# Kernel optimization log

Hardware: AMD Instinct MI355X
Metric: run time of the kernel (lower is better)

Reference implementation:

```python
import jax, jax.numpy as jnp
import numpy as np

B, S, D, H, IT, V = 2, 1024, 1024, 8, 28, 50257
DH = D // H
EPS = jnp.float32(1.1920929e-07)  # torch RMSNorm default eps = finfo(float32).eps


def _rmsnorm(x, w):
    # torch nn.RMSNorm: x * rsqrt(mean(x^2) + eps) * weight
    ms = jnp.mean(jnp.square(x), axis=-1, keepdims=True)
    return x * jax.lax.rsqrt(ms + EPS) * w


def setup_inputs() -> dict:
    key = jax.random.key(0)
    ks = jax.random.split(key, 8)
    s = 0.02
    tokens = jax.random.randint(ks[0], (B, S), 0, V)
    embed = jax.random.normal(ks[1], (V, D), dtype=jnp.float32) * s
    Wk = jax.random.normal(ks[2], (D, D), dtype=jnp.float32) * s
    Wv = jax.random.normal(ks[3], (D, D), dtype=jnp.float32) * s
    Ws = jax.random.normal(ks[4], (D, D), dtype=jnp.float32) * s
    Wo = jax.random.normal(ks[5], (D, D), dtype=jnp.float32) * s  # original zero-inits; randomized for a non-trivial baseline
    step_size = jnp.linspace(0.5, 0.1, IT, dtype=jnp.float32)
    norm_w = jnp.ones((IT, D), jnp.float32)   # per-iteration RMSNorm weight
    gamma = jnp.ones((IT, D), jnp.float32)
    beta = jnp.zeros((IT, D), jnp.float32)
    out_norm_w = jnp.ones((D,), jnp.float32)
    lm_head_w = jax.random.normal(ks[6], (V, D), dtype=jnp.float32) * s
    return dict(tokens=tokens, embed=embed, Wk=Wk, Wv=Wv, Ws=Ws, Wo=Wo,
                step_size=step_size, norm_w=norm_w, gamma=gamma, beta=beta,
                out_norm_w=out_norm_w, lm_head_w=lm_head_w)


def _forward(tokens, embed, Wk, Wv, Ws, Wo, step_size, norm_w, gamma, beta, out_norm_w, lm_head_w):
    b, s = tokens.shape
    causal = jnp.tril(jnp.ones((s, s), dtype=bool))  # allow j <= i
    scale = 1.0 / np.sqrt(DH)

    def compute_force(h):
        k = (h @ Wk.T).reshape(b, s, H, DH)
        v = (h @ Wv.T).reshape(b, s, H, DH)
        energy = jnp.einsum('bihd,bjhd->bhij', k, k) * scale
        logits = jnp.where(causal, -energy, -jnp.inf)  # softmax(-energy) with causal masking
        w = jax.nn.softmax(logits, axis=-1)
        pairwise = jnp.einsum('bhij,bjhd->bihd', w, v).reshape(b, s, D)
        return (pairwise + h @ Ws.T) @ Wo.T

    def step(x, p):
        st, nw, g, bb = p
        h = _rmsnorm(x, nw) * g + bb
        return x + compute_force(h) * st, None

    x0 = embed[tokens].astype(jnp.float32)
    x, _ = jax.lax.scan(jax.checkpoint(step), x0, (step_size, norm_w, gamma, beta))
    x = _rmsnorm(x, out_norm_w)
    return x @ lm_head_w.T  # [B, S, V] logits


def reference(tokens, embed, Wk, Wv, Ws, Wo, step_size, norm_w, gamma, beta, out_norm_w, lm_head_w):
    return _forward(tokens, embed, Wk, Wv, Ws, Wo, step_size, norm_w, gamma, beta, out_norm_w, lm_head_w)
```

## Files before the change

### kernel.cpp

```cpp
#include <hip/hip_runtime.h>
#include <cstdint>
#include <cstddef>

#define S_   1024
#define D_   1024
#define H_   8
#define DH_  128
#define IT_  28
#define V_   50257
#define B_   2
#define ROWS 2048
#define EPS_ 1.1920929e-07f

typedef unsigned short u16;
typedef __attribute__((ext_vector_type(8))) short s8v;
typedef __attribute__((ext_vector_type(4))) float f4v;

#define VMCNT0 asm volatile("s_waitcnt vmcnt(0)" ::: "memory")
#define RBAR   do { __builtin_amdgcn_s_barrier(); asm volatile("" ::: "memory"); } while (0)

static __device__ __forceinline__ void gload16(const void* g, void* l) {
  __builtin_amdgcn_global_load_lds((__attribute__((address_space(1))) void*)(g),
                                   (__attribute__((address_space(3))) void*)(l), 16, 0, 0);
}

static __device__ __forceinline__ u16 f2bf(float f) {
  union { float f; uint32_t u; } v; v.f = f;
  return (u16)((v.u + 0x7FFFu + ((v.u >> 16) & 1u)) >> 16);
}

static __device__ __forceinline__ float wave_sum(float v) {
#pragma unroll
  for (int o = 32; o > 0; o >>= 1) v += __shfl_xor(v, o, 64);
  return v;
}

__device__ __constant__ int IT_TAB[40] = {
  15,15,15,15, 14,14,14, 13,13,13, 12,12,12, 11,11,11,
  10,10, 9,9, 8,8, 7,7, 6, 5, 4, 3,
  14,10,6,2, 13,9,5,1, 12,8,4,0};
__device__ __constant__ int CH_TAB[40] = {
  0,1,2,3, 0,1,2, 0,1,2, 0,1,2, 0,1,2,
  0,1, 0,1, 0,1, 0,1, 0, 0, 0, 0,
  3,2,1,0, 3,2,1,0, 3,2,1,0};

__global__ __launch_bounds__(256) void k_embed(const int* __restrict__ tok,
                                               const float* __restrict__ emb,
                                               float* __restrict__ x) {
  const int row = blockIdx.x;
  const int t = tok[row];
  ((float4*)(x + (size_t)row * D_))[threadIdx.x] =
      ((const float4*)(emb + (size_t)t * D_))[threadIdx.x];
}

__global__ __launch_bounds__(256) void k_cvt(const float* __restrict__ w,
                                             u16* __restrict__ o, int n4) {
  const int idx = blockIdx.x * 256 + threadIdx.x;
  if (idx < n4) {
    const float4 f = ((const float4*)w)[idx];
    ushort4 u;
    u.x = f2bf(f.x); u.y = f2bf(f.y); u.z = f2bf(f.z); u.w = f2bf(f.w);
    ((ushort4*)o)[idx] = u;
  }
}

__global__ __launch_bounds__(256) void k_rmsnorm(const float* __restrict__ x,
                                                 const float* __restrict__ nw,
                                                 const float* __restrict__ g,
                                                 const float* __restrict__ bb,
                                                 u16* __restrict__ h) {
  const int row = blockIdx.x;
  const int tid = threadIdx.x;
  const float4 xv = ((const float4*)(x + (size_t)row * D_))[tid];
  float ss = xv.x*xv.x + xv.y*xv.y + xv.z*xv.z + xv.w*xv.w;
  ss = wave_sum(ss);
  __shared__ float red[4];
  const int lane = tid & 63, wid = tid >> 6;
  if (lane == 0) red[wid] = ss;
  __syncthreads();
  const float tot = red[0] + red[1] + red[2] + red[3];
  const float r = rsqrtf(tot * (1.0f / (float)D_) + EPS_);
  const float4 wv = ((const float4*)nw)[tid];
  float o[4];
  o[0] = xv.x * r * wv.x; o[1] = xv.y * r * wv.y;
  o[2] = xv.z * r * wv.z; o[3] = xv.w * r * wv.w;
  if (g) {
    const float4 gv = ((const float4*)g)[tid];
    const float4 bv = ((const float4*)bb)[tid];
    o[0] = o[0]*gv.x + bv.x; o[1] = o[1]*gv.y + bv.y;
    o[2] = o[2]*gv.z + bv.z; o[3] = o[3]*gv.w + bv.w;
  }
  ushort4 u;
  u.x = f2bf(o[0]); u.y = f2bf(o[1]); u.z = f2bf(o[2]); u.w = f2bf(o[3]);
  ((ushort4*)(h + (size_t)row * D_))[tid] = u;
}


__global__ __launch_bounds__(256) void k_gemm2(const u16* __restrict__ A, int lda,
                                               const u16* __restrict__ Bm, int ldb,
                                               float* __restrict__ C, int ldc,
                                               int K,
                                               const float* __restrict__ alphap, int aidx) {
  __shared__ u16 As0[128 * 32], As1[128 * 32];
  __shared__ u16 Bs0[64 * 32], Bs1[64 * 32];
  const int wk = (blockIdx.x & 7) * (gridDim.x >> 3) + (blockIdx.x >> 3);
  const int i0 = (wk & 15) * 128;
  const int j0 = (wk >> 4) * 64;
  const int tid = threadIdx.x;
  const int lane = tid & 63, w = tid >> 6;
  const int wr = w >> 1, wc = w & 1;
  const int l15 = lane & 15, l4 = lane >> 4;
  const int ar = tid >> 2;
  const int ak = (((tid & 3) ^ ((ar >> 1) & 3)) << 3);
  const int sw = (l15 >> 1) & 3;

  f4v acc[4][2];
#pragma unroll
  for (int m = 0; m < 4; ++m)
#pragma unroll
    for (int n = 0; n < 2; ++n) acc[m][n] = (f4v)0.0f;

  auto STAGE = [&](u16* AsB, u16* BsB, int k0) {
    gload16(A + (size_t)(i0 + ar) * lda + k0 + ak, AsB + (size_t)tid * 8);
    gload16(A + (size_t)(i0 + ar + 64) * lda + k0 + ak, AsB + ((size_t)tid + 256) * 8);
    gload16(Bm + (size_t)(j0 + ar) * ldb + k0 + ak, BsB + (size_t)tid * 8);
  };
  auto COMP = [&](const u16* AsB, const u16* BsB) {
    s8v a[4], b[2];
#pragma unroll
    for (int m = 0; m < 4; ++m)
      a[m] = *(const s8v*)&AsB[(wr * 64 + m * 16 + l15) * 32 + ((l4 ^ sw) << 3)];
#pragma unroll
    for (int n = 0; n < 2; ++n)
      b[n] = *(const s8v*)&BsB[(wc * 32 + n * 16 + l15) * 32 + ((l4 ^ sw) << 3)];
#pragma unroll
    for (int m = 0; m < 4; ++m)
#pragma unroll
      for (int n = 0; n < 2; ++n)
        acc[m][n] = __builtin_amdgcn_mfma_f32_16x16x32_bf16(a[m], b[n], acc[m][n], 0, 0, 0);
  };

  STAGE(As0, Bs0, 0);
  VMCNT0;
  RBAR;
  for (int k0 = 0; k0 < K; k0 += 64) {
    STAGE(As1, Bs1, k0 + 32);
    COMP(As0, Bs0);
    VMCNT0;
    RBAR;
    if (k0 + 64 < K) STAGE(As0, Bs0, k0 + 64);
    COMP(As1, Bs1);
    VMCNT0;
    RBAR;
  }

  const float alpha = alphap[aidx];
#pragma unroll
  for (int m = 0; m < 4; ++m) {
#pragma unroll
    for (int n = 0; n < 2; ++n) {
      const int i = i0 + wr * 64 + m * 16 + l4 * 4;
      const int j = j0 + wc * 32 + n * 16 + l15;
      const f4v v = acc[m][n];
#pragma unroll
      for (int r = 0; r < 4; ++r) C[(size_t)(i + r) * ldc + j] += alpha * v[r];
    }
  }
}

__global__ __launch_bounds__(256) void k_gemm_lm(const u16* __restrict__ A, int lda,
                                                 const u16* __restrict__ Bm, int ldb,
                                                 float* __restrict__ C, int ldc,
                                                 int N, int K) {
  __shared__ u16 As0[128 * 32], As1[128 * 32], As2[128 * 32];
  __shared__ u16 Bs0[128 * 32], Bs1[128 * 32], Bs2[128 * 32];
  const int per = gridDim.x >> 3;
  const int wk = (blockIdx.x & 7) * per + (blockIdx.x >> 3);
  const int i0 = (wk & 15) * 128;
  const int j0 = (wk >> 4) * 128;
  const int tid = threadIdx.x;
  const int lane = tid & 63, w = tid >> 6;
  const int wr = w >> 1, wc = w & 1;
  const int l15 = lane & 15, l4 = lane >> 4;
  const int ar = tid >> 2;
  const int ak = (((tid & 3) ^ ((ar >> 1) & 3)) << 3);
  const int sw = (l15 >> 1) & 3;
  int bj0 = j0 + ar;      if (bj0 > N - 1) bj0 = N - 1;
  int bj1 = j0 + ar + 64; if (bj1 > N - 1) bj1 = N - 1;

  f4v acc[4][4];
#pragma unroll
  for (int m = 0; m < 4; ++m)
#pragma unroll
    for (int n = 0; n < 4; ++n) acc[m][n] = (f4v)0.0f;

  auto STAGE = [&](u16* AsB, u16* BsB, int k0) {
    gload16(A + (size_t)(i0 + ar) * lda + k0 + ak, AsB + (size_t)tid * 8);
    gload16(A + (size_t)(i0 + ar + 64) * lda + k0 + ak, AsB + ((size_t)tid + 256) * 8);
    gload16(Bm + (size_t)bj0 * ldb + k0 + ak, BsB + (size_t)tid * 8);
    gload16(Bm + (size_t)bj1 * ldb + k0 + ak, BsB + ((size_t)tid + 256) * 8);
  };
  auto COMP = [&](const u16* AsB, const u16* BsB) {
    s8v a[4], b[4];
#pragma unroll
    for (int m = 0; m < 4; ++m)
      a[m] = *(const s8v*)&AsB[(wr * 64 + m * 16 + l15) * 32 + ((l4 ^ sw) << 3)];
#pragma unroll
    for (int n = 0; n < 4; ++n)
      b[n] = *(const s8v*)&BsB[(wc * 64 + n * 16 + l15) * 32 + ((l4 ^ sw) << 3)];
#pragma unroll
    for (int m = 0; m < 4; ++m)
#pragma unroll
      for (int n = 0; n < 4; ++n)
        acc[m][n] = __builtin_amdgcn_mfma_f32_16x16x32_bf16(a[m], b[n], acc[m][n], 0, 0, 0);
  };
  auto WAIT = [&](int ahead) {
    if (ahead >= 2)      asm volatile("s_waitcnt vmcnt(8)" ::: "memory");
    else if (ahead == 1) asm volatile("s_waitcnt vmcnt(4)" ::: "memory");
    else                 VMCNT0;
  };

  const int nk = K >> 5;
  STAGE(As0, Bs0, 0);
  STAGE(As1, Bs1, 32);
  STAGE(As2, Bs2, 64);
  for (int i = 0; i < nk; ++i) {
    u16 *Asb, *Bsb;
    const int m3 = i % 3;
    if (m3 == 0) { Asb = As0; Bsb = Bs0; }
    else if (m3 == 1) { Asb = As1; Bsb = Bs1; }
    else { Asb = As2; Bsb = Bs2; }
    const int rem = nk - 1 - i;
    WAIT(rem < 2 ? rem : 2);
    RBAR;
    COMP(Asb, Bsb);
    RBAR;
    if (i + 3 < nk) STAGE(Asb, Bsb, (i + 3) << 5);
  }

#pragma unroll
  for (int m = 0; m < 4; ++m) {
#pragma unroll
    for (int n = 0; n < 4; ++n) {
      const int i = i0 + wr * 64 + m * 16 + l4 * 4;
      const int j = j0 + wc * 64 + n * 16 + l15;
      const f4v v = acc[m][n];
      if (j < N) {
#pragma unroll
        for (int r = 0; r < 4; ++r) C[(size_t)(i + r) * ldc + j] = v[r];
      }
    }
  }
}

__global__ __launch_bounds__(256) void k_gemm_qkv(const u16* __restrict__ A,
                                                  const u16* __restrict__ Wcat,
                                                  u16* __restrict__ kb,
                                                  u16* __restrict__ vt,
                                                  float* __restrict__ fb) {
  __shared__ u16 As0[128 * 32], As1[128 * 32];
  __shared__ u16 Bs0[64 * 32], Bs1[64 * 32];
  const int wk = (blockIdx.x & 7) * (gridDim.x >> 3) + (blockIdx.x >> 3);
  const int i0 = (wk & 15) * 128;
  const int j0 = (wk >> 4) * 64;
  const int tid = threadIdx.x;
  const int lane = tid & 63, w = tid >> 6;
  const int wr = w >> 1, wc = w & 1;
  const int l15 = lane & 15, l4 = lane >> 4;
  const int ar = tid >> 2;
  const int ak = (((tid & 3) ^ ((ar >> 1) & 3)) << 3);
  const int sw = (l15 >> 1) & 3;

  f4v acc[4][2];
#pragma unroll
  for (int m = 0; m < 4; ++m)
#pragma unroll
    for (int n = 0; n < 2; ++n) acc[m][n] = (f4v)0.0f;

  auto STAGE = [&](u16* AsB, u16* BsB, int k0) {
    gload16(A + (size_t)(i0 + ar) * D_ + k0 + ak, AsB + (size_t)tid * 8);
    gload16(A + (size_t)(i0 + ar + 64) * D_ + k0 + ak, AsB + ((size_t)tid + 256) * 8);
    gload16(Wcat + (size_t)(j0 + ar) * D_ + k0 + ak, BsB + (size_t)tid * 8);
  };
  auto COMP = [&](const u16* AsB, const u16* BsB) {
    s8v a[4], b[2];
#pragma unroll
    for (int m = 0; m < 4; ++m)
      a[m] = *(const s8v*)&AsB[(wr * 64 + m * 16 + l15) * 32 + ((l4 ^ sw) << 3)];
#pragma unroll
    for (int n = 0; n < 2; ++n)
      b[n] = *(const s8v*)&BsB[(wc * 32 + n * 16 + l15) * 32 + ((l4 ^ sw) << 3)];
#pragma unroll
    for (int m = 0; m < 4; ++m)
#pragma unroll
      for (int n = 0; n < 2; ++n)
        acc[m][n] = __builtin_amdgcn_mfma_f32_16x16x32_bf16(a[m], b[n], acc[m][n], 0, 0, 0);
  };

  STAGE(As0, Bs0, 0);
  VMCNT0;
  RBAR;
  for (int k0 = 0; k0 < D_; k0 += 64) {
    STAGE(As1, Bs1, k0 + 32);
    COMP(As0, Bs0);
    VMCNT0;
    RBAR;
    if (k0 + 64 < D_) STAGE(As0, Bs0, k0 + 64);
    COMP(As1, Bs1);
    VMCNT0;
    RBAR;
  }

#pragma unroll
  for (int m = 0; m < 4; ++m) {
#pragma unroll
    for (int n = 0; n < 2; ++n) {
      const int i = i0 + wr * 64 + m * 16 + l4 * 4;
      const int j = j0 + wc * 32 + n * 16 + l15;
      const int sel = j >> 10, jl = j & 1023;
      const f4v v = acc[m][n];
      if (sel == 0) {
#pragma unroll
        for (int r = 0; r < 4; ++r) kb[(size_t)(i + r) * D_ + jl] = f2bf(v[r]);
      } else if (sel == 1) {
        ushort4 p;
        p.x = f2bf(v[0]); p.y = f2bf(v[1]); p.z = f2bf(v[2]); p.w = f2bf(v[3]);
        *(ushort4*)&vt[((size_t)(i >> 10) * D_ + jl) * S_ + (i & 1023)] = p;
      } else {
#pragma unroll
        for (int r = 0; r < 4; ++r) fb[(size_t)(i + r) * D_ + jl] = v[r];
      }
    }
  }
}

__global__ __launch_bounds__(256) void k_attn_part(const u16* __restrict__ kb,
                                                   const u16* __restrict__ vt,
                                                   float* __restrict__ po,
                                                   float* __restrict__ pml,
                                                   float scale) {
  const int it = IT_TAB[blockIdx.x], ch = CH_TAB[blockIdx.x];
  const int z = blockIdx.y;
  const int b = z >> 3, h = z & 7;
  const u16* Kbh = kb + (size_t)b * S_ * D_ + h * DH_;
  const u16* Vth = vt + ((size_t)b * D_ + h * DH_) * S_;
  const int i0 = it * 64;
  const int jt0 = ch * 4;
  const int jtend = min(jt0 + 4, it + 1);
  __shared__ u16 Kj[64 * 128];
  __shared__ u16 Vj[128 * 64];
  __shared__ u16 Pl[4][16 * 64];
  const int tid = threadIdx.x;
  const int lane = tid & 63, w = tid >> 6;
  const int l15 = lane & 15, l4 = lane >> 4;

  s8v ka[4];
#pragma unroll
  for (int ks = 0; ks < 4; ++ks)
    ka[ks] = *(const s8v*)(Kbh + (size_t)(i0 + w * 16 + l15) * D_ + ks * 32 + l4 * 8);

  f4v acc_o[8];
#pragma unroll
  for (int n = 0; n < 8; ++n) acc_o[n] = (f4v)0.0f;
  float mrow[4], lrow[4];
#pragma unroll
  for (int r = 0; r < 4; ++r) { mrow[r] = -3.0e38f; lrow[r] = 0.f; }

  const int krow = tid >> 4, koff = (tid & 15) * 8;
  const int vrow = tid >> 3, voff = (tid & 7) * 8;

  for (int jt = jt0; jt < jtend; ++jt) {
    const int j0 = jt * 64;
#pragma unroll
    for (int p = 0; p < 4; ++p) {
      const int row = p * 16 + krow;
      gload16(Kbh + (size_t)(j0 + row) * D_ + (koff ^ ((row & 7) << 3)),
              &Kj[(size_t)(p * 256 + tid) * 8]);
    }
#pragma unroll
    for (int p = 0; p < 4; ++p) {
      const int row = p * 32 + vrow;
      gload16(Vth + (size_t)row * S_ + j0 + (voff ^ ((row & 7) << 3)),
              &Vj[(size_t)(p * 256 + tid) * 8]);
    }
    __syncthreads();

    f4v s[4];
#pragma unroll
    for (int n = 0; n < 4; ++n) s[n] = (f4v)0.0f;
    __builtin_amdgcn_s_setprio(1);
#pragma unroll
    for (int ks = 0; ks < 4; ++ks) {
#pragma unroll
      for (int n = 0; n < 4; ++n) {
        const int row = n * 16 + l15;
        const s8v kf = *(const s8v*)&Kj[row * 128 + ((ks * 32 + l4 * 8) ^ ((row & 7) << 3))];
        s[n] = __builtin_amdgcn_mfma_f32_16x16x32_bf16(ka[ks], kf, s[n], 0, 0, 0);
      }
    }
    __builtin_amdgcn_s_setprio(0);

    float pv[4][4], tmax[4];
#pragma unroll
    for (int r = 0; r < 4; ++r) tmax[r] = -3.0e38f;
#pragma unroll
    for (int n = 0; n < 4; ++n) {
      const int j = j0 + n * 16 + l15;
#pragma unroll
      for (int r = 0; r < 4; ++r) {
        const int i = i0 + w * 16 + l4 * 4 + r;
        const float lg = (j <= i) ? (-scale * s[n][r]) : -3.0e38f;
        pv[n][r] = lg;
        tmax[r] = fmaxf(tmax[r], lg);
      }
    }
#pragma unroll
    for (int r = 0; r < 4; ++r) {
#pragma unroll
      for (int o = 8; o > 0; o >>= 1) tmax[r] = fmaxf(tmax[r], __shfl_xor(tmax[r], o, 64));
    }
    float es[4];
#pragma unroll
    for (int r = 0; r < 4; ++r) {
      const float mn = fmaxf(mrow[r], tmax[r]);
      es[r] = __expf(mrow[r] - mn);
      mrow[r] = mn;
    }
    float psum[4] = {0.f, 0.f, 0.f, 0.f};
#pragma unroll
    for (int n = 0; n < 4; ++n) {
#pragma unroll
      for (int r = 0; r < 4; ++r) {
        const float p = __expf(pv[n][r] - mrow[r]);
        pv[n][r] = p;
        psum[r] += p;
      }
    }
#pragma unroll
    for (int r = 0; r < 4; ++r) {
#pragma unroll
      for (int o = 8; o > 0; o >>= 1) psum[r] += __shfl_xor(psum[r], o, 64);
      lrow[r] = lrow[r] * es[r] + psum[r];
    }
#pragma unroll
    for (int n = 0; n < 8; ++n) {
      f4v t = acc_o[n];
      t[0] *= es[0]; t[1] *= es[1]; t[2] *= es[2]; t[3] *= es[3];
      acc_o[n] = t;
    }

    u16* P = Pl[w];
#pragma unroll
    for (int n = 0; n < 4; ++n) {
#pragma unroll
      for (int r = 0; r < 4; ++r) {
        const int row = l4 * 4 + r;
        P[row * 64 + ((n * 16 + l15) ^ ((row & 7) << 3))] = f2bf(pv[n][r]);
      }
    }
    __syncthreads();
    s8v pa[2];
#pragma unroll
    for (int kp = 0; kp < 2; ++kp)
      pa[kp] = *(const s8v*)&P[l15 * 64 + ((kp * 32 + l4 * 8) ^ ((l15 & 7) << 3))];

    __builtin_amdgcn_s_setprio(1);
#pragma unroll
    for (int kp = 0; kp < 2; ++kp) {
#pragma unroll
      for (int n = 0; n < 8; ++n) {
        const int d = n * 16 + l15;
        const s8v vf = *(const s8v*)&Vj[d * 64 + ((kp * 32 + l4 * 8) ^ ((d & 7) << 3))];
        acc_o[n] = __builtin_amdgcn_mfma_f32_16x16x32_bf16(pa[kp], vf, acc_o[n], 0, 0, 0);
      }
    }
    __builtin_amdgcn_s_setprio(0);
    __syncthreads();
  }

  const int slot = (z * 16 + it) * 4 + ch;
  float* O = po + (size_t)slot * (64 * 128);
#pragma unroll
  for (int n = 0; n < 8; ++n) {
#pragma unroll
    for (int r = 0; r < 4; ++r)
      O[(w * 16 + l4 * 4 + r) * 128 + n * 16 + l15] = acc_o[n][r];
  }
  if (l15 == 0) {
#pragma unroll
    for (int r = 0; r < 4; ++r) {
      const int row = w * 16 + l4 * 4 + r;
      pml[(size_t)slot * 128 + row] = mrow[r];
      pml[(size_t)slot * 128 + 64 + row] = lrow[r];
    }
  }
}

__global__ __launch_bounds__(256) void k_attn_merge(const float* __restrict__ po,
                                                    const float* __restrict__ pml,
                                                    const float* __restrict__ fb,
                                                    u16* __restrict__ fbh) {
  const int it = blockIdx.x, z = blockIdx.y;
  const int b = z >> 3, h = z & 7;
  const int nch = (it >> 2) + 1;
  const int row = threadIdx.x >> 2;
  const int cseg = (threadIdx.x & 3) * 32;
  const int base = (z * 16 + it) * 4;

  float ms = -3.0e38f, mv[4], lv[4];
#pragma unroll
  for (int c = 0; c < 4; ++c)
    if (c < nch) {
      mv[c] = pml[(size_t)(base + c) * 128 + row];
      lv[c] = pml[(size_t)(base + c) * 128 + 64 + row];
      ms = fmaxf(ms, mv[c]);
    }
  float ls = 0.f, fac[4];
#pragma unroll
  for (int c = 0; c < 4; ++c)
    if (c < nch) { fac[c] = __expf(mv[c] - ms); ls += lv[c] * fac[c]; }
  const float inv = 1.0f / ls;

  float4 o[8];
#pragma unroll
  for (int q = 0; q < 8; ++q) o[q] = make_float4(0.f, 0.f, 0.f, 0.f);
#pragma unroll
  for (int c = 0; c < 4; ++c)
    if (c < nch) {
      const float4* Oc = (const float4*)(po + (size_t)(base + c) * (64 * 128) + row * 128 + cseg);
      const float f = fac[c];
#pragma unroll
      for (int q = 0; q < 8; ++q) {
        const float4 t = Oc[q];
        o[q].x += t.x * f; o[q].y += t.y * f; o[q].z += t.z * f; o[q].w += t.w * f;
      }
    }

  const size_t gidx = ((size_t)(b * S_ + it * 64 + row)) * D_ + h * DH_ + cseg;
  const float4* F = (const float4*)(fb + gidx);
  u16* out = fbh + gidx;
#pragma unroll
  for (int q = 0; q < 8; ++q) {
    const float4 fv = F[q];
    ushort4 u;
    u.x = f2bf(fv.x + o[q].x * inv);
    u.y = f2bf(fv.y + o[q].y * inv);
    u.z = f2bf(fv.z + o[q].z * inv);
    u.w = f2bf(fv.w + o[q].w * inv);
    *(ushort4*)(out + q * 4) = u;
  }
}

extern "C" void kernel_launch(void* const* d_in, const int* in_sizes, int n_in,
                              void* d_out, int out_size, void* d_ws, size_t ws_size,
                              hipStream_t stream) {
  const int*   tok = (const int*)  d_in[0];
  const float* emb = (const float*)d_in[1];
  const float* Wk  = (const float*)d_in[2];
  const float* Wv  = (const float*)d_in[3];
  const float* Ws  = (const float*)d_in[4];
  const float* Wo  = (const float*)d_in[5];
  const float* stp = (const float*)d_in[6];
  const float* nw  = (const float*)d_in[7];
  const float* gam = (const float*)d_in[8];
  const float* bet = (const float*)d_in[9];
  const float* onw = (const float*)d_in[10];
  const float* lmw = (const float*)d_in[11];
  float* out = (float*)d_out;

  uint8_t* wsb = (uint8_t*)d_ws;
  float* x   = (float*)wsb;  wsb += (size_t)ROWS * D_ * 4;
  u16* hb    = (u16*)wsb;    wsb += (size_t)ROWS * D_ * 2;
  u16* kb    = (u16*)wsb;    wsb += (size_t)ROWS * D_ * 2;
  u16* vt    = (u16*)wsb;    wsb += (size_t)ROWS * D_ * 2;
  float* fb  = (float*)wsb;  wsb += (size_t)ROWS * D_ * 4;
  u16* fbh   = (u16*)wsb;    wsb += (size_t)ROWS * D_ * 2;
  u16* Wcat  = (u16*)wsb;    wsb += (size_t)3 * D_ * D_ * 2;
  u16* Wob   = (u16*)wsb;    wsb += (size_t)D_ * D_ * 2;
  float* po  = (float*)wsb;  wsb += (size_t)1024 * 64 * 128 * 4;
  float* pml = (float*)wsb;  wsb += (size_t)1024 * 128 * 4;
  u16* Wlm   = (u16*)wsb;    wsb += (size_t)V_ * D_ * 2;

  const float scale = 0.08838834764831845f;
  const int n4 = D_ * D_ / 4;

  k_cvt<<<1024, 256, 0, stream>>>(Wk, Wcat, n4);
  k_cvt<<<1024, 256, 0, stream>>>(Wv, Wcat + (size_t)D_ * D_, n4);
  k_cvt<<<1024, 256, 0, stream>>>(Ws, Wcat + (size_t)2 * D_ * D_, n4);
  k_cvt<<<1024, 256, 0, stream>>>(Wo, Wob, n4);
  k_embed<<<ROWS, 256, 0, stream>>>(tok, emb, x);

  for (int it = 0; it < IT_; ++it) {
    k_rmsnorm<<<ROWS, 256, 0, stream>>>(x, nw + (size_t)it * D_,
                                        gam + (size_t)it * D_, bet + (size_t)it * D_, hb);
    k_gemm_qkv<<<768, 256, 0, stream>>>(hb, Wcat, kb, vt, fb);
    k_attn_part<<<dim3(40, 16), 256, 0, stream>>>(kb, vt, po, pml, scale);
    k_attn_merge<<<dim3(16, 16), 256, 0, stream>>>(po, pml, fb, fbh);
    k_gemm2<<<256, 256, 0, stream>>>(fbh, D_, Wob, D_, x, D_, D_, stp, it);
  }

  k_rmsnorm<<<ROWS, 256, 0, stream>>>(x, onw, nullptr, nullptr, hb);

  k_cvt<<<(V_ * 256 + 255) / 256, 256, 0, stream>>>(lmw, Wlm, V_ * D_ / 4);
  k_gemm_lm<<<16 * ((V_ + 127) / 128), 256, 0, stream>>>(hb, D_, Wlm, D_, out, V_, V_, D_);
}
```

Measured before the change: 2.731 ms.

## Double-buffer K/V tiles in attention partial kernel and drop mid-loop barrier

```diff
diff --git a/kernel.cpp b/kernel.cpp
--- a/kernel.cpp
+++ b/kernel.cpp
@@ -17,6 +17,7 @@
 typedef __attribute__((ext_vector_type(4))) float f4v;
 
 #define VMCNT0 asm volatile("s_waitcnt vmcnt(0)" ::: "memory")
+#define LGKM0  asm volatile("s_waitcnt lgkmcnt(0)" ::: "memory")
 #define RBAR   do { __builtin_amdgcn_s_barrier(); asm volatile("" ::: "memory"); } while (0)
 
 static __device__ __forceinline__ void gload16(const void* g, void* l) {
@@ -347,8 +348,8 @@
   const int i0 = it * 64;
   const int jt0 = ch * 4;
   const int jtend = min(jt0 + 4, it + 1);
-  __shared__ u16 Kj[64 * 128];
-  __shared__ u16 Vj[128 * 64];
+  __shared__ u16 Kj[2][64 * 128];
+  __shared__ u16 Vj[2][128 * 64];
   __shared__ u16 Pl[4][16 * 64];
   const int tid = threadIdx.x;
   const int lane = tid & 63, w = tid >> 6;
@@ -369,21 +370,33 @@
   const int krow = tid >> 4, koff = (tid & 15) * 8;
   const int vrow = tid >> 3, voff = (tid & 7) * 8;
 
+  auto stageKV = [&](int j0g, int bi) {
+    u16* Kd = Kj[bi];
+    u16* Vd = Vj[bi];
+#pragma unroll
+    for (int p = 0; p < 4; ++p) {
+      const int row = p * 16 + krow;
+      gload16(Kbh + (size_t)(j0g + row) * D_ + (koff ^ ((row & 7) << 3)),
+              Kd + (size_t)(p * 256 + tid) * 8);
+    }
+#pragma unroll
+    for (int p = 0; p < 4; ++p) {
+      const int row = p * 32 + vrow;
+      gload16(Vth + (size_t)row * S_ + j0g + (voff ^ ((row & 7) << 3)),
+              Vd + (size_t)(p * 256 + tid) * 8);
+    }
+  };
+
+  stageKV(jt0 * 64, 0);
+  VMCNT0;
+  RBAR;
+
+  int cur = 0;
   for (int jt = jt0; jt < jtend; ++jt) {
     const int j0 = jt * 64;
-#pragma unroll
-    for (int p = 0; p < 4; ++p) {
-      const int row = p * 16 + krow;
-      gload16(Kbh + (size_t)(j0 + row) * D_ + (koff ^ ((row & 7) << 3)),
-              &Kj[(size_t)(p * 256 + tid) * 8]);
-    }
-#pragma unroll
-    for (int p = 0; p < 4; ++p) {
-      const int row = p * 32 + vrow;
-      gload16(Vth + (size_t)row * S_ + j0 + (voff ^ ((row & 7) << 3)),
-              &Vj[(size_t)(p * 256 + tid) * 8]);
-    }
-    __syncthreads();
+    if (jt + 1 < jtend) stageKV((jt + 1) * 64, cur ^ 1);
+    const u16* Kc = Kj[cur];
+    const u16* Vc = Vj[cur];
 
     f4v s[4];
 #pragma unroll
@@ -394,7 +407,7 @@
 #pragma unroll
       for (int n = 0; n < 4; ++n) {
         const int row = n * 16 + l15;
-        const s8v kf = *(const s8v*)&Kj[row * 128 + ((ks * 32 + l4 * 8) ^ ((row & 7) << 3))];
+        const s8v kf = *(const s8v*)&Kc[row * 128 + ((ks * 32 + l4 * 8) ^ ((row & 7) << 3))];
         s[n] = __builtin_amdgcn_mfma_f32_16x16x32_bf16(ka[ks], kf, s[n], 0, 0, 0);
       }
     }
@@ -458,7 +471,8 @@
         P[row * 64 + ((n * 16 + l15) ^ ((row & 7) << 3))] = f2bf(pv[n][r]);
       }
     }
-    __syncthreads();
+    LGKM0;
+    __builtin_amdgcn_sched_barrier(0);
     s8v pa[2];
 #pragma unroll
     for (int kp = 0; kp < 2; ++kp)
@@ -470,12 +484,15 @@
 #pragma unroll
       for (int n = 0; n < 8; ++n) {
         const int d = n * 16 + l15;
-        const s8v vf = *(const s8v*)&Vj[d * 64 + ((kp * 32 + l4 * 8) ^ ((d & 7) << 3))];
+        const s8v vf = *(const s8v*)&Vc[d * 64 + ((kp * 32 + l4 * 8) ^ ((d & 7) << 3))];
         acc_o[n] = __builtin_amdgcn_mfma_f32_16x16x32_bf16(pa[kp], vf, acc_o[n], 0, 0, 0);
       }
     }
     __builtin_amdgcn_s_setprio(0);
-    __syncthreads();
+
+    VMCNT0;
+    RBAR;
+    cur ^= 1;
   }
 
   const int slot = (z * 16 + it) * 4 + ch;
```

Result: no change. 2.763 ms (+1.1%).
